# Performance work log

Hardware: AMD Instinct MI355X
Metric: run time of the kernel (lower is better)

The kernel has to match this reference:

```python
import jax, jax.numpy as jnp
import numpy as np

T = 2048          # num tokens (single prefill sequence)
H = 32            # num local heads
HIDDEN = 5120
Q_LORA = 1536
KV_LORA = 512
D_NOPE = 128
D_ROPE = 64
D_QK = D_NOPE + D_ROPE   # 192
D_V = 128
EPS = 1e-6
SCALING = D_QK ** -0.5


def _rope_tables(theta=10000.0):
    inv_freq = 1.0 / (theta ** (np.arange(0, D_ROPE, 2, dtype=np.float32) / D_ROPE))
    t = np.arange(T, dtype=np.float32)
    freqs = np.outer(t, inv_freq)                       # [T, D_ROPE/2]
    emb = np.concatenate([freqs, freqs], axis=-1)       # [T, D_ROPE]
    return (jnp.asarray(np.cos(emb))[:, None, :],       # [T,1,D_ROPE]
            jnp.asarray(np.sin(emb))[:, None, :])


def setup_inputs() -> dict:
    key = jax.random.key(0)
    ks = jax.random.split(key, 6)
    cos, sin = _rope_tables()
    s = lambda fan_in: 1.0 / np.sqrt(fan_in)
    return {
        'hidden_states': jax.random.normal(ks[0], (T, HIDDEN), jnp.float32),
        'cos': cos,
        'sin': sin,
        'wq_a': jax.random.normal(ks[1], (HIDDEN, Q_LORA), jnp.float32) * s(HIDDEN),
        'q_a_ln_w': jnp.ones((Q_LORA,), jnp.float32),
        'wq_b': jax.random.normal(ks[2], (Q_LORA, H * D_QK), jnp.float32) * s(Q_LORA),
        'wkv_a': jax.random.normal(ks[3], (HIDDEN, KV_LORA + D_ROPE), jnp.float32) * s(HIDDEN),
        'kv_a_ln_w': jnp.ones((KV_LORA,), jnp.float32),
        'wkv_b': jax.random.normal(ks[4], (KV_LORA, H * (D_NOPE + D_V)), jnp.float32) * s(KV_LORA),
        'wo': jax.random.normal(ks[5], (H * D_V, HIDDEN), jnp.float32) * s(H * D_V),
    }


def _rmsnorm(x, w):
    var = jnp.mean(jnp.square(x), axis=-1, keepdims=True)
    return x * jax.lax.rsqrt(var + EPS) * w


def _deinterleave(x):
    # torch: x.view(..., d//2, 2).transpose(-1,-2).reshape(..., d)
    return jnp.concatenate([x[..., 0::2], x[..., 1::2]], axis=-1)


def _rotate_half(x):
    h = x.shape[-1] // 2
    return jnp.concatenate([-x[..., h:], x[..., :h]], axis=-1)


def _apply_rope(q, k, cos, sin):
    q = _deinterleave(q)
    k = _deinterleave(k)
    return q * cos + _rotate_half(q) * sin, k * cos + _rotate_half(k) * sin


def reference(hidden_states, cos, sin, wq_a, q_a_ln_w, wq_b, wkv_a, kv_a_ln_w, wkv_b, wo):
    # Q path: low-rank down-proj, RMSNorm, up-proj
    q = _rmsnorm(hidden_states @ wq_a, q_a_ln_w) @ wq_b
    q = q.reshape(T, H, D_QK)
    q_nope, q_pe = q[..., :D_NOPE], q[..., D_NOPE:]

    # KV path: joint compressed latent + rope key slice
    ckv = hidden_states @ wkv_a
    compressed, k_pe = ckv[..., :KV_LORA], ckv[..., KV_LORA:].reshape(T, 1, D_ROPE)
    kv = (_rmsnorm(compressed, kv_a_ln_w) @ wkv_b).reshape(T, H, D_NOPE + D_V)
    k_nope, value = kv[..., :D_NOPE], kv[..., D_NOPE:]

    # split RoPE on the rope sub-dims only
    q_pe, k_pe = _apply_rope(q_pe, k_pe, cos, sin)
    q = jnp.concatenate([q_nope, q_pe], axis=-1)                    # [T,H,192]
    k = jnp.concatenate([k_nope, jnp.broadcast_to(k_pe, (T, H, D_ROPE))], axis=-1)

    # causal attention (prefill)
    scores = jnp.einsum('qhd,khd->hqk', q, k) * SCALING             # [H,T,T]
    mask = jnp.tril(jnp.ones((T, T), bool))
    scores = jnp.where(mask[None], scores, jnp.finfo(scores.dtype).min)
    probs = jax.nn.softmax(scores, axis=-1)
    attn = jnp.einsum('hqk,khd->qhd', probs, value)                 # [T,H,128]

    return attn.reshape(T, H * D_V) @ wo                            # [T,HIDDEN]
```

## Files before the change

kernel.cpp:

```cpp
#include <hip/hip_runtime.h>
#include <hip/hip_bf16.h>
#include <stdint.h>

typedef __hip_bfloat16 bf16;
typedef short v8s __attribute__((ext_vector_type(8)));
typedef float v4f __attribute__((ext_vector_type(4)));

#define T_SEQ 2048
#define NH 32
#define HIDDEN_D 5120
#define QL 1536
#define KVL 512
#define DQK 192
#define DV 128
#define NAB 2176
#define SCALE_QK 0.07216878364870322f

static __device__ __forceinline__ float b2f(bf16 x) { return __bfloat162float(x); }
static __device__ __forceinline__ bf16 f2b(float x) { return __float2bfloat16(x); }
static __device__ __forceinline__ unsigned short bbits(bf16 x) {
  union { bf16 b; unsigned short u; } c; c.b = x; return c.u;
}

#define AS1(p) ((__attribute__((address_space(1))) void*)(p))
#define AS3(p) ((__attribute__((address_space(3))) void*)(p))

__global__ void detect_k(const void* __restrict__ lnw, int* __restrict__ flag) {
  if (threadIdx.x == 0 && blockIdx.x == 0) {
    uint32_t u = *(const uint32_t*)lnw;
    flag[0] = ((u & 0xFFFFu) == 0x3F80u) ? 1 : 0;
  }
}

__global__ __launch_bounds__(256) void conv_bf16(const void* __restrict__ in,
        bf16* __restrict__ out, const int* __restrict__ flag, int n4) {
  int i = blockIdx.x * 256 + threadIdx.x;
  if (i >= n4) return;
  if (flag[0]) {
    ((uint2*)out)[i] = ((const uint2*)in)[i];
  } else {
    float4 v = ((const float4*)in)[i];
    uint2 o;
    o.x = ((uint32_t)bbits(f2b(v.y)) << 16) | bbits(f2b(v.x));
    o.y = ((uint32_t)bbits(f2b(v.w)) << 16) | bbits(f2b(v.z));
    ((uint2*)out)[i] = o;
  }
}

__global__ __launch_bounds__(256) void transpose_any(const void* __restrict__ in,
        bf16* __restrict__ out, int R, int C, int Cpad, const int* __restrict__ flag) {
  __shared__ unsigned short tile[32][33];
  const int isb = flag[0];
  int c0 = blockIdx.x * 32, r0 = blockIdx.y * 32;
  int tx = threadIdx.x, ty = threadIdx.y;
#pragma unroll
  for (int i = 0; i < 32; i += 8) {
    unsigned short v = 0;
    int c = c0 + tx;
    if (c < C) {
      size_t idx = (size_t)(r0 + ty + i) * C + c;
      v = isb ? *((const unsigned short*)in + idx)
              : bbits(f2b(((const float*)in)[idx]));
    }
    tile[ty + i][tx] = v;
  }
  __syncthreads();
#pragma unroll
  for (int i = 0; i < 32; i += 8) {
    int c = c0 + ty + i;
    if (c < Cpad) *(unsigned short*)&out[(size_t)c * R + r0 + tx] = tile[tx][ty + i];
  }
}

template <bool FINAL>
__global__ __launch_bounds__(256, 2)
void gemm_bt(const bf16* __restrict__ A, const bf16* __restrict__ Bt,
             void* __restrict__ C, const int* __restrict__ flag,
             int M, int N, int K) {
  __shared__ __align__(16) bf16 As[128 * 64];
  __shared__ __align__(16) bf16 Bs[128 * 64];
  const int tid = threadIdx.x;
  const int wv = tid >> 6;
  const int lane = tid & 63;
  const int quad = lane >> 4;
  const int c16 = lane & 15;
  const int wm = (wv & 1) * 64;
  const int wn = (wv >> 1) * 64;
  const int m0 = blockIdx.y * 128;
  const int n0 = blockIdx.x * 128;

  v4f acc[4][4] = {};

  const int sr = tid >> 3;
  const int sc = (((tid & 7) ^ (sr & 7)) << 3);

  for (int k0 = 0; k0 < K; k0 += 64) {
    __syncthreads();
#pragma unroll
    for (int i = 0; i < 4; ++i) {
      const bf16* ga = A  + (size_t)(m0 + i * 32 + sr) * K + k0 + sc;
      const bf16* gb = Bt + (size_t)(n0 + i * 32 + sr) * K + k0 + sc;
      __builtin_amdgcn_global_load_lds(AS1(ga), AS3(As + (i * 256 + tid) * 8), 16, 0, 0);
      __builtin_amdgcn_global_load_lds(AS1(gb), AS3(Bs + (i * 256 + tid) * 8), 16, 0, 0);
    }
    __syncthreads();
#pragma unroll
    for (int ks = 0; ks < 2; ++ks) {
      v8s af[4], bfr[4];
#pragma unroll
      for (int t = 0; t < 4; ++t) {
        int ra = wm + t * 16 + c16;
        af[t]  = *(const v8s*)(As + ra * 64 + (((ks * 4 + quad) ^ (ra & 7)) << 3));
        int rb = wn + t * 16 + c16;
        bfr[t] = *(const v8s*)(Bs + rb * 64 + (((ks * 4 + quad) ^ (rb & 7)) << 3));
      }
#pragma unroll
      for (int i = 0; i < 4; ++i)
#pragma unroll
        for (int j = 0; j < 4; ++j)
          acc[i][j] = __builtin_amdgcn_mfma_f32_16x16x32_bf16(af[i], bfr[j], acc[i][j], 0, 0, 0);
    }
  }
  const bool outBf = FINAL ? (flag[0] != 0) : true;
#pragma unroll
  for (int i = 0; i < 4; ++i)
#pragma unroll
    for (int j = 0; j < 4; ++j) {
      int m = m0 + wm + i * 16 + quad * 4;
      int n = n0 + wn + j * 16 + c16;
#pragma unroll
      for (int r = 0; r < 4; ++r) {
        if (outBf) ((bf16*)C)[(size_t)(m + r) * N + n] = f2b(acc[i][j][r]);
        else       ((float*)C)[(size_t)(m + r) * N + n] = acc[i][j][r];
      }
    }
}

template <int N>
__global__ __launch_bounds__(256) void rmsnorm_k(const bf16* __restrict__ in,
        const void* __restrict__ w, const int* __restrict__ flag,
        bf16* __restrict__ out, int strideIn, int strideOut) {
  constexpr int CNT = N / 256;
  const int row = blockIdx.x, tid = threadIdx.x;
  const int isb = flag[0];
  const bf16* x = in + (size_t)row * strideIn;
  float v[CNT];
  float ss = 0.f;
#pragma unroll
  for (int i = 0; i < CNT; ++i) { v[i] = b2f(x[tid + i * 256]); ss += v[i] * v[i]; }
#pragma unroll
  for (int o = 32; o > 0; o >>= 1) ss += __shfl_xor(ss, o);
  __shared__ float wsum[4];
  if ((tid & 63) == 0) wsum[tid >> 6] = ss;
  __syncthreads();
  float scale = rsqrtf((wsum[0] + wsum[1] + wsum[2] + wsum[3]) / (float)N + 1e-6f);
#pragma unroll
  for (int i = 0; i < CNT; ++i) {
    int c = tid + i * 256;
    float wv = isb ? b2f(((const bf16*)w)[c]) : ((const float*)w)[c];
    out[(size_t)row * strideOut + c] = f2b(v[i] * scale * wv);
  }
}

__global__ __launch_bounds__(256) void qk_build(const bf16* __restrict__ qraw,
        const bf16* __restrict__ ckv, const bf16* __restrict__ kv,
        const void* __restrict__ cosb, const void* __restrict__ sinb,
        const int* __restrict__ flag,
        bf16* __restrict__ Qh, bf16* __restrict__ Kh) {
  const int t = blockIdx.x, tid = threadIdx.x;
  const int isb = flag[0];
  __shared__ float cs[64], sn[64], kpe[64];
  if (tid < 64) {
    int j = tid;
    float c = isb ? b2f(((const bf16*)cosb)[t * 64 + j]) : ((const float*)cosb)[t * 64 + j];
    float s = isb ? b2f(((const bf16*)sinb)[t * 64 + j]) : ((const float*)sinb)[t * 64 + j];
    cs[j] = c; sn[j] = s;
    const bf16* kp = ckv + (size_t)t * NAB + 512;
    float v;
    if (j < 32) v = b2f(kp[2 * j]) * c - b2f(kp[2 * j + 1]) * s;
    else { int i2 = j - 32; v = b2f(kp[2 * i2 + 1]) * c + b2f(kp[2 * i2]) * s; }
    kpe[j] = v;
  }
  __syncthreads();
  for (int idx = tid; idx < 512; idx += 256) {
    int h = idx >> 4, d8 = (idx & 15) * 8;
    *(uint4*)&Qh[((size_t)h * T_SEQ + t) * DQK + d8] =
        *(const uint4*)&qraw[(size_t)t * 6144 + h * DQK + d8];
    *(uint4*)&Kh[((size_t)h * T_SEQ + t) * DQK + d8] =
        *(const uint4*)&kv[(size_t)t * 8192 + h * 256 + d8];
  }
  for (int idx = tid; idx < 2048; idx += 256) {
    int h = idx >> 6, j = idx & 63;
    const bf16* qp = qraw + (size_t)t * 6144 + h * DQK + 128;
    float v;
    if (j < 32) v = b2f(qp[2 * j]) * cs[j] - b2f(qp[2 * j + 1]) * sn[j];
    else { int i2 = j - 32; v = b2f(qp[2 * i2 + 1]) * cs[j] + b2f(qp[2 * i2]) * sn[j]; }
    Qh[((size_t)h * T_SEQ + t) * DQK + 128 + j] = f2b(v);
    Kh[((size_t)h * T_SEQ + t) * DQK + 128 + j] = f2b(kpe[j]);
  }
}

__global__ __launch_bounds__(256) void vt_build(const bf16* __restrict__ kv,
                                                bf16* __restrict__ VT) {
  __shared__ unsigned short tile[32][33];
  int h = blockIdx.z;
  int t0 = blockIdx.x * 32, d0 = blockIdx.y * 32;
  int tx = threadIdx.x, ty = threadIdx.y;
#pragma unroll
  for (int i = 0; i < 32; i += 8)
    tile[ty + i][tx] = *(const unsigned short*)
        &kv[(size_t)(t0 + ty + i) * 8192 + h * 256 + 128 + d0 + tx];
  __syncthreads();
#pragma unroll
  for (int i = 0; i < 32; i += 8)
    *(unsigned short*)&VT[((size_t)h * DV + d0 + ty + i) * T_SEQ + t0 + tx] = tile[tx][ty + i];
}

__global__ __launch_bounds__(256, 2)
void mla_attn(const bf16* __restrict__ Qh, const bf16* __restrict__ Kh,
              const bf16* __restrict__ VT, bf16* __restrict__ attn) {
  const int wg = blockIdx.x + blockIdx.y * 16;
  const int swz = (wg & 7) * 64 + (wg >> 3);
  const int pid = swz & 15, h = swz >> 4;
  const int tid = threadIdx.x, wv = tid >> 6, lane = tid & 63;
  const int quad = lane >> 4, c16 = lane & 15;

  __shared__ __align__(16) bf16 Ksh[64 * 200];
  __shared__ __align__(16) bf16 Vsh[128 * 72];
  __shared__ __align__(16) bf16 Psh[4 * 16 * 72];
  bf16* pw = Psh + wv * (16 * 72);

#pragma unroll 1
  for (int pass = 0; pass < 2; ++pass) {
    const int qt = (pass == 0) ? pid : (31 - pid);
    const int qbase = qt * 64;

    v8s qf[6];
    {
      const bf16* qp = Qh + ((size_t)h * T_SEQ + qbase + wv * 16 + c16) * DQK;
#pragma unroll
      for (int ks = 0; ks < 6; ++ks) qf[ks] = *(const v8s*)(qp + ks * 32 + quad * 8);
    }

    v4f oacc[8] = {};
    float mrow[4] = {-1e30f, -1e30f, -1e30f, -1e30f};
    float lrow[4] = {0.f, 0.f, 0.f, 0.f};

    for (int kt = 0; kt <= qt; ++kt) {
      const int kb = kt * 64;
      __syncthreads();
      for (int c = tid; c < 1536; c += 256) {
        int r = c / 24, off = (c % 24) * 8;
        *(uint4*)(Ksh + r * 200 + off) =
            *(const uint4*)(Kh + ((size_t)h * T_SEQ + kb + r) * DQK + off);
      }
      for (int c = tid; c < 1024; c += 256) {
        int r = c >> 3, off = (c & 7) * 8;
        *(uint4*)(Vsh + r * 72 + off) =
            *(const uint4*)(VT + ((size_t)h * DV + r) * T_SEQ + kb + off);
      }
      __syncthreads();

      v4f sacc[4] = {};
#pragma unroll
      for (int nt = 0; nt < 4; ++nt)
#pragma unroll
        for (int ks = 0; ks < 6; ++ks) {
          v8s kf = *(const v8s*)(Ksh + (nt * 16 + c16) * 200 + ks * 32 + quad * 8);
          sacc[nt] = __builtin_amdgcn_mfma_f32_16x16x32_bf16(qf[ks], kf, sacc[nt], 0, 0, 0);
        }

      float rmax[4] = {-1e30f, -1e30f, -1e30f, -1e30f};
      const int rowg = qbase + wv * 16 + quad * 4;
#pragma unroll
      for (int nt = 0; nt < 4; ++nt) {
        int col = kb + nt * 16 + c16;
#pragma unroll
        for (int r = 0; r < 4; ++r) {
          float s = sacc[nt][r] * SCALE_QK;
          if (col > rowg + r) s = -1e30f;
          sacc[nt][r] = s;
          rmax[r] = fmaxf(rmax[r], s);
        }
      }
#pragma unroll
      for (int r = 0; r < 4; ++r)
#pragma unroll
        for (int o = 8; o > 0; o >>= 1) rmax[r] = fmaxf(rmax[r], __shfl_xor(rmax[r], o));

      float alpha[4], rsum[4];
#pragma unroll
      for (int r = 0; r < 4; ++r) {
        float mnew = fmaxf(mrow[r], rmax[r]);
        alpha[r] = __expf(mrow[r] - mnew);
        mrow[r] = mnew;
        rsum[r] = 0.f;
      }
#pragma unroll
      for (int nt = 0; nt < 4; ++nt)
#pragma unroll
        for (int r = 0; r < 4; ++r) {
          float p = __expf(sacc[nt][r] - mrow[r]);
          sacc[nt][r] = p;
          rsum[r] += p;
        }
#pragma unroll
      for (int r = 0; r < 4; ++r) {
#pragma unroll
        for (int o = 8; o > 0; o >>= 1) rsum[r] += __shfl_xor(rsum[r], o);
        lrow[r] = lrow[r] * alpha[r] + rsum[r];
      }
#pragma unroll
      for (int i = 0; i < 8; ++i)
#pragma unroll
        for (int r = 0; r < 4; ++r) oacc[i][r] *= alpha[r];

#pragma unroll
      for (int nt = 0; nt < 4; ++nt)
#pragma unroll
        for (int r = 0; r < 4; ++r)
          pw[(quad * 4 + r) * 72 + nt * 16 + c16] = f2b(sacc[nt][r]);

#pragma unroll
      for (int ks = 0; ks < 2; ++ks) {
        v8s paf = *(const v8s*)(pw + c16 * 72 + ks * 32 + quad * 8);
#pragma unroll
        for (int nt = 0; nt < 8; ++nt) {
          v8s vf = *(const v8s*)(Vsh + (nt * 16 + c16) * 72 + ks * 32 + quad * 8);
          oacc[nt] = __builtin_amdgcn_mfma_f32_16x16x32_bf16(paf, vf, oacc[nt], 0, 0, 0);
        }
      }
    }

#pragma unroll
    for (int r = 0; r < 4; ++r) {
      float inv = 1.f / lrow[r];
      int trow = qbase + wv * 16 + quad * 4 + r;
#pragma unroll
      for (int nt = 0; nt < 8; ++nt)
        attn[(size_t)trow * 4096 + h * DV + nt * 16 + c16] = f2b(oacc[nt][r] * inv);
    }
  }
}

extern "C" void kernel_launch(void* const* d_in, const int* in_sizes, int n_in,
                              void* d_out, int out_size, void* d_ws, size_t ws_size,
                              hipStream_t stream) {
  (void)in_sizes; (void)n_in; (void)out_size; (void)ws_size;
  const void* hidden   = d_in[0];
  const void* cosb     = d_in[1];
  const void* sinb     = d_in[2];
  const void* wq_a     = d_in[3];
  const void* q_a_ln_w = d_in[4];
  const void* wq_b     = d_in[5];
  const void* wkv_a    = d_in[6];
  const void* kv_a_ln_w= d_in[7];
  const void* wkv_b    = d_in[8];
  const void* wo       = d_in[9];

  int* flag = (int*)d_ws;
  bf16* ws  = (bf16*)d_ws + 16;

  size_t o = 0;
  bf16* wqaT  = ws + o; o += (size_t)QL * HIDDEN_D;
  bf16* wkvaT = ws + o; o += (size_t)640 * HIDDEN_D;
  bf16* wqbT  = ws + o; o += (size_t)6144 * QL;
  bf16* wkvbT = ws + o; o += (size_t)8192 * KVL;
  bf16* woT   = ws + o; o += (size_t)HIDDEN_D * 4096;
  bf16* Hb    = ws + o; o += (size_t)T_SEQ * HIDDEN_D;
  bf16* Cab   = ws + o; o += (size_t)T_SEQ * NAB;
  bf16* q_raw = ws + o; o += (size_t)T_SEQ * 6144;
  bf16* attn  = q_raw;
  bf16* kv    = ws + o; o += (size_t)T_SEQ * 8192;
  bf16* Qh    = ws + o; o += (size_t)NH * T_SEQ * DQK;
  bf16* Kh    = ws + o; o += (size_t)NH * T_SEQ * DQK;
  bf16* VT    = ws + o; o += (size_t)NH * DV * T_SEQ;
  bf16* q_a_n = Qh;
  bf16* ckv_n = Qh + (size_t)T_SEQ * QL;

  detect_k<<<1, 64, 0, stream>>>(q_a_ln_w, flag);

  conv_bf16<<<(T_SEQ * HIDDEN_D / 4 + 255) / 256, 256, 0, stream>>>(hidden, Hb, flag,
                                                                    T_SEQ * HIDDEN_D / 4);
  dim3 b32(32, 8);
  transpose_any<<<dim3(1536/32, 5120/32), b32, 0, stream>>>(wq_a,  wqaT, 5120, 1536, 1536, flag);
  transpose_any<<<dim3(6144/32, 1536/32), b32, 0, stream>>>(wq_b,  wqbT, 1536, 6144, 6144, flag);
  transpose_any<<<dim3(640/32,  5120/32), b32, 0, stream>>>(wkv_a, wkvaT, 5120, 576, 640, flag);
  transpose_any<<<dim3(8192/32, 512/32),  b32, 0, stream>>>(wkv_b, wkvbT, 512, 8192, 8192, flag);
  transpose_any<<<dim3(5120/32, 4096/32), b32, 0, stream>>>(wo,    woT, 4096, 5120, 5120, flag);

  gemm_bt<false><<<dim3(NAB/128, 16), 256, 0, stream>>>(Hb, wqaT, Cab, flag, T_SEQ, NAB, HIDDEN_D);
  rmsnorm_k<1536><<<T_SEQ, 256, 0, stream>>>(Cab, q_a_ln_w, flag, q_a_n, NAB, 1536);
  gemm_bt<false><<<dim3(6144/128, 16), 256, 0, stream>>>(q_a_n, wqbT, q_raw, flag, T_SEQ, 6144, 1536);
  rmsnorm_k<512><<<T_SEQ, 256, 0, stream>>>(Cab + QL, kv_a_ln_w, flag, ckv_n, NAB, 512);
  gemm_bt<false><<<dim3(8192/128, 16), 256, 0, stream>>>(ckv_n, wkvbT, kv, flag, T_SEQ, 8192, 512);

  qk_build<<<T_SEQ, 256, 0, stream>>>(q_raw, Cab + QL, kv, cosb, sinb, flag, Qh, Kh);
  vt_build<<<dim3(T_SEQ/32, DV/32, NH), b32, 0, stream>>>(kv, VT);
  mla_attn<<<dim3(16, NH), 256, 0, stream>>>(Qh, Kh, VT, attn);

  gemm_bt<true><<<dim3(5120/128, 16), 256, 0, stream>>>(attn, woT, d_out, flag, T_SEQ, 5120, 4096);
}
```

Measured before the change: 836.9 us.

## Split attention into one block per query tile with lazy softmax rescaling

The attention kernel now launches one workgroup per (head, query tile), 1024 in total, instead of pairing two query tiles per workgroup. Heavy tiles are ordered first so the scheduler can balance the causal workload. It also adds exp2-based softmax with the scale folded in, applies the causal mask only on the diagonal tile, and skips the running-max rescale of accumulators unless the max grows by more than a threshold. Load balance now depends on hardware scheduling order rather than explicit pairing, and the lazy rescale relies on bounded growth to stay numerically safe.

```diff
diff --git a/kernel.cpp b/kernel.cpp
--- a/kernel.cpp
+++ b/kernel.cpp
@@ -15,6 +15,7 @@
 #define DV 128
 #define NAB 2176
 #define SCALE_QK 0.07216878364870322f
+#define SCALE_LOG2 0.10411754f
 
 static __device__ __forceinline__ float b2f(bf16 x) { return __bfloat162float(x); }
 static __device__ __forceinline__ bf16 f2b(float x) { return __float2bfloat16(x); }
@@ -219,9 +220,10 @@
 __global__ __launch_bounds__(256, 2)
 void mla_attn(const bf16* __restrict__ Qh, const bf16* __restrict__ Kh,
               const bf16* __restrict__ VT, bf16* __restrict__ attn) {
-  const int wg = blockIdx.x + blockIdx.y * 16;
-  const int swz = (wg & 7) * 64 + (wg >> 3);
-  const int pid = swz & 15, h = swz >> 4;
+  const int wg = blockIdx.x + blockIdx.y * 32;
+  const int swz = (wg & 7) * 128 + (wg >> 3);
+  const int h = swz >> 5;
+  const int qt = 31 - (swz & 31);
   const int tid = threadIdx.x, wv = tid >> 6, lane = tid & 63;
   const int quad = lane >> 4, c16 = lane & 15;
 
@@ -230,116 +232,121 @@
   __shared__ __align__(16) bf16 Psh[4 * 16 * 72];
   bf16* pw = Psh + wv * (16 * 72);
 
-#pragma unroll 1
-  for (int pass = 0; pass < 2; ++pass) {
-    const int qt = (pass == 0) ? pid : (31 - pid);
-    const int qbase = qt * 64;
-
-    v8s qf[6];
-    {
-      const bf16* qp = Qh + ((size_t)h * T_SEQ + qbase + wv * 16 + c16) * DQK;
-#pragma unroll
-      for (int ks = 0; ks < 6; ++ks) qf[ks] = *(const v8s*)(qp + ks * 32 + quad * 8);
-    }
-
-    v4f oacc[8] = {};
-    float mrow[4] = {-1e30f, -1e30f, -1e30f, -1e30f};
-    float lrow[4] = {0.f, 0.f, 0.f, 0.f};
-
-    for (int kt = 0; kt <= qt; ++kt) {
-      const int kb = kt * 64;
-      __syncthreads();
-      for (int c = tid; c < 1536; c += 256) {
-        int r = c / 24, off = (c % 24) * 8;
-        *(uint4*)(Ksh + r * 200 + off) =
-            *(const uint4*)(Kh + ((size_t)h * T_SEQ + kb + r) * DQK + off);
-      }
-      for (int c = tid; c < 1024; c += 256) {
-        int r = c >> 3, off = (c & 7) * 8;
-        *(uint4*)(Vsh + r * 72 + off) =
-            *(const uint4*)(VT + ((size_t)h * DV + r) * T_SEQ + kb + off);
-      }
-      __syncthreads();
-
-      v4f sacc[4] = {};
-#pragma unroll
-      for (int nt = 0; nt < 4; ++nt)
-#pragma unroll
-        for (int ks = 0; ks < 6; ++ks) {
-          v8s kf = *(const v8s*)(Ksh + (nt * 16 + c16) * 200 + ks * 32 + quad * 8);
-          sacc[nt] = __builtin_amdgcn_mfma_f32_16x16x32_bf16(qf[ks], kf, sacc[nt], 0, 0, 0);
-        }
-
-      float rmax[4] = {-1e30f, -1e30f, -1e30f, -1e30f};
-      const int rowg = qbase + wv * 16 + quad * 4;
+  const int qbase = qt * 64;
+
+  v8s qf[6];
+  {
+    const bf16* qp = Qh + ((size_t)h * T_SEQ + qbase + wv * 16 + c16) * DQK;
+#pragma unroll
+    for (int ks = 0; ks < 6; ++ks) qf[ks] = *(const v8s*)(qp + ks * 32 + quad * 8);
+  }
+
+  v4f oacc[8] = {};
+  float mrow[4] = {-1e30f, -1e30f, -1e30f, -1e30f};
+  float lrow[4] = {0.f, 0.f, 0.f, 0.f};
+  const int rowg = qbase + wv * 16 + quad * 4;
+
+  for (int kt = 0; kt <= qt; ++kt) {
+    const int kb = kt * 64;
+    __syncthreads();
+    for (int c = tid; c < 1536; c += 256) {
+      int r = c / 24, off = (c % 24) * 8;
+      *(uint4*)(Ksh + r * 200 + off) =
+          *(const uint4*)(Kh + ((size_t)h * T_SEQ + kb + r) * DQK + off);
+    }
+    for (int c = tid; c < 1024; c += 256) {
+      int r = c >> 3, off = (c & 7) * 8;
+      *(uint4*)(Vsh + r * 72 + off) =
+          *(const uint4*)(VT + ((size_t)h * DV + r) * T_SEQ + kb + off);
+    }
+    __syncthreads();
+
+    v4f sacc[4] = {};
+#pragma unroll
+    for (int nt = 0; nt < 4; ++nt)
+#pragma unroll
+      for (int ks = 0; ks < 6; ++ks) {
+        v8s kf = *(const v8s*)(Ksh + (nt * 16 + c16) * 200 + ks * 32 + quad * 8);
+        sacc[nt] = __builtin_amdgcn_mfma_f32_16x16x32_bf16(qf[ks], kf, sacc[nt], 0, 0, 0);
+      }
+
+#pragma unroll
+    for (int nt = 0; nt < 4; ++nt)
+#pragma unroll
+      for (int r = 0; r < 4; ++r) sacc[nt][r] *= SCALE_LOG2;
+    if (kt == qt) {
 #pragma unroll
       for (int nt = 0; nt < 4; ++nt) {
         int col = kb + nt * 16 + c16;
 #pragma unroll
-        for (int r = 0; r < 4; ++r) {
-          float s = sacc[nt][r] * SCALE_QK;
-          if (col > rowg + r) s = -1e30f;
-          sacc[nt][r] = s;
-          rmax[r] = fmaxf(rmax[r], s);
-        }
-      }
-#pragma unroll
-      for (int r = 0; r < 4; ++r)
-#pragma unroll
-        for (int o = 8; o > 0; o >>= 1) rmax[r] = fmaxf(rmax[r], __shfl_xor(rmax[r], o));
-
-      float alpha[4], rsum[4];
+        for (int r = 0; r < 4; ++r)
+          if (col > rowg + r) sacc[nt][r] = -1e30f;
+      }
+    }
+    float rmax[4] = {-1e30f, -1e30f, -1e30f, -1e30f};
+#pragma unroll
+    for (int nt = 0; nt < 4; ++nt)
+#pragma unroll
+      for (int r = 0; r < 4; ++r) rmax[r] = fmaxf(rmax[r], sacc[nt][r]);
+#pragma unroll
+    for (int r = 0; r < 4; ++r)
+#pragma unroll
+      for (int o = 8; o > 0; o >>= 1) rmax[r] = fmaxf(rmax[r], __shfl_xor(rmax[r], o));
+
+    int need = (rmax[0] > mrow[0] + 8.f) | (rmax[1] > mrow[1] + 8.f) |
+               (rmax[2] > mrow[2] + 8.f) | (rmax[3] > mrow[3] + 8.f);
+    if (__any(need)) {
 #pragma unroll
       for (int r = 0; r < 4; ++r) {
         float mnew = fmaxf(mrow[r], rmax[r]);
-        alpha[r] = __expf(mrow[r] - mnew);
+        float alpha = exp2f(mrow[r] - mnew);
         mrow[r] = mnew;
-        rsum[r] = 0.f;
-      }
-#pragma unroll
-      for (int nt = 0; nt < 4; ++nt)
-#pragma unroll
-        for (int r = 0; r < 4; ++r) {
-          float p = __expf(sacc[nt][r] - mrow[r]);
-          sacc[nt][r] = p;
-          rsum[r] += p;
-        }
+        lrow[r] *= alpha;
+#pragma unroll
+        for (int i = 0; i < 8; ++i) oacc[i][r] *= alpha;
+      }
+    }
+
+    float rsum[4] = {0.f, 0.f, 0.f, 0.f};
+#pragma unroll
+    for (int nt = 0; nt < 4; ++nt)
 #pragma unroll
       for (int r = 0; r < 4; ++r) {
-#pragma unroll
-        for (int o = 8; o > 0; o >>= 1) rsum[r] += __shfl_xor(rsum[r], o);
-        lrow[r] = lrow[r] * alpha[r] + rsum[r];
-      }
-#pragma unroll
-      for (int i = 0; i < 8; ++i)
-#pragma unroll
-        for (int r = 0; r < 4; ++r) oacc[i][r] *= alpha[r];
-
-#pragma unroll
-      for (int nt = 0; nt < 4; ++nt)
-#pragma unroll
-        for (int r = 0; r < 4; ++r)
-          pw[(quad * 4 + r) * 72 + nt * 16 + c16] = f2b(sacc[nt][r]);
-
-#pragma unroll
-      for (int ks = 0; ks < 2; ++ks) {
-        v8s paf = *(const v8s*)(pw + c16 * 72 + ks * 32 + quad * 8);
-#pragma unroll
-        for (int nt = 0; nt < 8; ++nt) {
-          v8s vf = *(const v8s*)(Vsh + (nt * 16 + c16) * 72 + ks * 32 + quad * 8);
-          oacc[nt] = __builtin_amdgcn_mfma_f32_16x16x32_bf16(paf, vf, oacc[nt], 0, 0, 0);
-        }
-      }
-    }
-
+        float p = exp2f(sacc[nt][r] - mrow[r]);
+        sacc[nt][r] = p;
+        rsum[r] += p;
+      }
 #pragma unroll
     for (int r = 0; r < 4; ++r) {
-      float inv = 1.f / lrow[r];
-      int trow = qbase + wv * 16 + quad * 4 + r;
-#pragma unroll
-      for (int nt = 0; nt < 8; ++nt)
-        attn[(size_t)trow * 4096 + h * DV + nt * 16 + c16] = f2b(oacc[nt][r] * inv);
-    }
+#pragma unroll
+      for (int o = 8; o > 0; o >>= 1) rsum[r] += __shfl_xor(rsum[r], o);
+      lrow[r] += rsum[r];
+    }
+
+#pragma unroll
+    for (int nt = 0; nt < 4; ++nt)
+#pragma unroll
+      for (int r = 0; r < 4; ++r)
+        pw[(quad * 4 + r) * 72 + nt * 16 + c16] = f2b(sacc[nt][r]);
+
+#pragma unroll
+    for (int ks = 0; ks < 2; ++ks) {
+      v8s paf = *(const v8s*)(pw + c16 * 72 + ks * 32 + quad * 8);
+#pragma unroll
+      for (int nt = 0; nt < 8; ++nt) {
+        v8s vf = *(const v8s*)(Vsh + (nt * 16 + c16) * 72 + ks * 32 + quad * 8);
+        oacc[nt] = __builtin_amdgcn_mfma_f32_16x16x32_bf16(paf, vf, oacc[nt], 0, 0, 0);
+      }
+    }
+  }
+
+#pragma unroll
+  for (int r = 0; r < 4; ++r) {
+    float inv = 1.f / lrow[r];
+    int trow = qbase + wv * 16 + quad * 4 + r;
+#pragma unroll
+    for (int nt = 0; nt < 8; ++nt)
+      attn[(size_t)trow * 4096 + h * DV + nt * 16 + c16] = f2b(oacc[nt][r] * inv);
   }
 }
 
@@ -397,7 +404,7 @@
 
   qk_build<<<T_SEQ, 256, 0, stream>>>(q_raw, Cab + QL, kv, cosb, sinb, flag, Qh, Kh);
   vt_build<<<dim3(T_SEQ/32, DV/32, NH), b32, 0, stream>>>(kv, VT);
-  mla_attn<<<dim3(16, NH), 256, 0, stream>>>(Qh, Kh, VT, attn);
+  mla_attn<<<dim3(32, NH), 256, 0, stream>>>(Qh, Kh, VT, attn);
 
   gemm_bt<true><<<dim3(5120/128, 16), 256, 0, stream>>>(attn, woT, d_out, flag, T_SEQ, 5120, 4096);
 }
```

Measured after the change: 858.0 us. +2.5%, slower.
